# Performance work log

Hardware: AMD Instinct MI355X
Metric: run time of the kernel (lower is better)

## Reference

```python
import jax, jax.numpy as jnp
import numpy as np

N, E, G, F_IN, H, C = 50000, 800000, 512, 128, 96, 10
BN_EPS = 1e-5


def _bn(x, w, b):
    # torch BatchNorm1d training-mode forward: batch stats, biased variance
    mu = jnp.mean(x, axis=0)
    var = jnp.var(x, axis=0)
    return (x - mu) * jax.lax.rsqrt(var + BN_EPS) * w + b


def setup_inputs() -> dict:
    key = jax.random.key(0)
    ks = iter(jax.random.split(key, 64))

    def rn(shape, s=0.05):
        return jax.random.normal(next(ks), shape, jnp.float32) * s

    inp = {
        "x": jax.random.normal(next(ks), (N, F_IN), jnp.float32),
        "edge_index": jax.random.randint(next(ks), (2, E), 0, N, dtype=jnp.int32),
        "batch": jnp.sort(jax.random.randint(next(ks), (N,), 0, G, dtype=jnp.int32)),
        "bn_feat_w": jnp.ones((F_IN,), jnp.float32),
        "bn_feat_b": jnp.full((F_IN,), 1e-4, jnp.float32),
        "Wf": rn((F_IN, H)), "bf": jnp.zeros((H,), jnp.float32),
        "bn_fc_w": jnp.ones((H,), jnp.float32),
        "bn_fc_b": jnp.full((H,), 1e-4, jnp.float32),
        "Wl": rn((H, H)), "bl": jnp.zeros((H,), jnp.float32),
        "bn_hid_w": jnp.ones((H,), jnp.float32),
        "bn_hid_b": jnp.full((H,), 1e-4, jnp.float32),
        "Wc": rn((H, C)), "bc": jnp.zeros((C,), jnp.float32),
    }
    for i in range(3):
        inp[f"W1_{i}"] = rn((H, H)); inp[f"b1_{i}"] = jnp.zeros((H,), jnp.float32)
        inp[f"bnw_{i}"] = jnp.ones((H,), jnp.float32)
        inp[f"bnb_{i}"] = jnp.full((H,), 1e-4, jnp.float32)
        inp[f"W2_{i}"] = rn((H, H)); inp[f"b2_{i}"] = jnp.zeros((H,), jnp.float32)
    return inp


def reference(x, edge_index, batch, bn_feat_w, bn_feat_b, Wf, bf,
              W1_0, b1_0, bnw_0, bnb_0, W2_0, b2_0,
              W1_1, b1_1, bnw_1, bnb_1, W2_1, b2_1,
              W1_2, b1_2, bnw_2, bnb_2, W2_2, b2_2,
              bn_fc_w, bn_fc_b, Wl, bl, bn_hid_w, bn_hid_b, Wc, bc):
    src, dst = edge_index[0], edge_index[1]
    h = _bn(x, bn_feat_w, bn_feat_b)
    # GCNConv(gfn=True): pure linear feature transform, no propagation
    h = jax.nn.relu(h @ Wf + bf)
    gin_params = [
        (W1_0, b1_0, bnw_0, bnb_0, W2_0, b2_0),
        (W1_1, b1_1, bnw_1, bnb_1, W2_1, b2_1),
        (W1_2, b1_2, bnw_2, bnb_2, W2_2, b2_2),
    ]
    for W1, b1, bw, bb, W2, b2 in gin_params:
        # GIN: (1+eps)*x + sum-aggregate of neighbor features (eps=0)
        agg = jax.ops.segment_sum(h[src], dst, num_segments=N)  # [N, H]
        m = h + agg
        m = jax.nn.relu(_bn(m @ W1 + b1, bw, bb))
        h = jax.nn.relu(m @ W2 + b2)
    # global_add_pool over graphs
    g = jax.ops.segment_sum(h, batch, num_segments=G)  # [G, H]
    g = jax.nn.relu(_bn(g, bn_fc_w, bn_fc_b) @ Wl + bl)
    g = _bn(g, bn_hid_w, bn_hid_b)
    logits = g @ Wc + bc
    return jax.nn.log_softmax(logits, axis=-1)
```

## Files before the change

### kernel.cpp

```cpp
#include <hip/hip_runtime.h>

#define N_NODES 50000
#define N_EDGES 800000
#define N_GRAPHS 512
#define F_IN 128
#define HDIM 96
#define NCLS 10
#define BN_EPS 1e-5f

#define NPB 128
#define NBUCK2 ((N_NODES + NPB - 1) / NPB)
#define NEB 128
#define EPB ((N_EDGES + NEB - 1) / NEB)

typedef unsigned int u32;
typedef unsigned short u16;
typedef __attribute__((ext_vector_type(8))) short bf16x8;
typedef __attribute__((ext_vector_type(4))) float f32x4;

__device__ __forceinline__ u16 f2bf(float f) {
    u32 u = __float_as_uint(f);
    u32 r = (u + 0x7fffu + ((u >> 16) & 1u)) >> 16;
    return (u16)r;
}
__device__ __forceinline__ float bflo(u32 w) { return __uint_as_float(w << 16); }
__device__ __forceinline__ float bfhi(u32 w) { return __uint_as_float(w & 0xffff0000u); }
__device__ __forceinline__ float bf2f(u16 v) { return __uint_as_float((u32)v << 16); }

template<int NC>
__global__ __launch_bounds__(256) void colstats4_kernel(const float* __restrict__ in,
                                                        float* __restrict__ partials,
                                                        int nrows) {
    constexpr int CG  = NC / 4;
    constexpr int RPB = 256 / CG;
    const int cg = threadIdx.x % CG;
    const int rg = threadIdx.x / CG;
    float4 s = make_float4(0.f, 0.f, 0.f, 0.f);
    float4 q = make_float4(0.f, 0.f, 0.f, 0.f);
    for (int r = blockIdx.x * RPB + rg; r < nrows; r += gridDim.x * RPB) {
        float4 v = *(const float4*)&in[(size_t)r * NC + cg * 4];
        s.x += v.x; s.y += v.y; s.z += v.z; s.w += v.w;
        q.x += v.x * v.x; q.y += v.y * v.y; q.z += v.z * v.z; q.w += v.w * v.w;
    }
    __shared__ float ss[RPB][NC], sq[RPB][NC];
    *(float4*)&ss[rg][cg * 4] = s;
    *(float4*)&sq[rg][cg * 4] = q;
    __syncthreads();
    if (threadIdx.x < NC) {
        float a = 0.f, b = 0.f;
        #pragma unroll
        for (int r = 0; r < RPB; r++) { a += ss[r][threadIdx.x]; b += sq[r][threadIdx.x]; }
        partials[(size_t)blockIdx.x * 2 * NC + threadIdx.x]      = a;
        partials[(size_t)blockIdx.x * 2 * NC + NC + threadIdx.x] = b;
    }
}

template<int NC>
__global__ __launch_bounds__(2*NC) void colstats_kernel(const float* __restrict__ in,
                                                        float* __restrict__ partials,
                                                        int nrows) {
    const int col  = threadIdx.x % NC;
    const int half = threadIdx.x / NC;
    float s = 0.f, ss = 0.f;
    for (int r = blockIdx.x * 2 + half; r < nrows; r += gridDim.x * 2) {
        float v = in[(size_t)r * NC + col];
        s += v; ss += v * v;
    }
    __shared__ float shs[2][NC], shq[2][NC];
    shs[half][col] = s; shq[half][col] = ss;
    __syncthreads();
    if (half == 0) {
        partials[(size_t)blockIdx.x * 2 * NC + col]      = s  + shs[1][col];
        partials[(size_t)blockIdx.x * 2 * NC + NC + col] = ss + shq[1][col];
    }
}

template<int NCOLS>
__global__ __launch_bounds__(NCOLS * 8) void reduce_finalize_kernel(
        const float* __restrict__ partials, int nslots,
        const float* __restrict__ w,
        const float* __restrict__ b,
        float* __restrict__ ac, float inv_n) {
    const int k   = threadIdx.x % NCOLS;
    const int grp = threadIdx.x / NCOLS;
    const int stride = 2 * NCOLS;
    float s = 0.f, q = 0.f;
    for (int i = grp; i < nslots; i += 8) {
        s += partials[(size_t)i * stride + k];
        q += partials[(size_t)i * stride + NCOLS + k];
    }
    __shared__ float ss[8][NCOLS], sq[8][NCOLS];
    ss[grp][k] = s; sq[grp][k] = q;
    __syncthreads();
    if (grp == 0) {
        float S = ((ss[0][k] + ss[1][k]) + (ss[2][k] + ss[3][k]))
                + ((ss[4][k] + ss[5][k]) + (ss[6][k] + ss[7][k]));
        float Q = ((sq[0][k] + sq[1][k]) + (sq[2][k] + sq[3][k]))
                + ((sq[4][k] + sq[5][k]) + (sq[6][k] + sq[7][k]));
        float mu  = S * inv_n;
        float var = Q * inv_n - mu * mu;
        float a   = w[k] * rsqrtf(var + BN_EPS);
        ac[k]         = a;
        ac[NCOLS + k] = b[k] - mu * a;
    }
}

#define WPF_BLOCKS 48
#define WPH_BLOCKS 36
__global__ __launch_bounds__(256) void wprep_all_kernel(
        const float* __restrict__ Wf, const float* __restrict__ bf, const float* __restrict__ acX,
        const float* __restrict__ W0a, const float* __restrict__ b0a,
        const float* __restrict__ W0b, const float* __restrict__ b0b,
        const float* __restrict__ W1a, const float* __restrict__ b1a,
        const float* __restrict__ W1b, const float* __restrict__ b1b,
        const float* __restrict__ W2a, const float* __restrict__ b2a,
        const float* __restrict__ W2b, const float* __restrict__ b2b,
        u16* __restrict__ wtF, float* __restrict__ bFm,
        u16* __restrict__ wtbase, float* __restrict__ bmbase) {
    const int tid = threadIdx.x;
    int blk = blockIdx.x;
    if (blk < WPF_BLOCKS) {
        int i = blk * 256 + tid;
        if (i < F_IN * 96) {
            int k = i / 96, n = i % 96;
            wtF[n * F_IN + k] = f2bf(Wf[i] * acX[k]);
        }
        if (blk == 0 && tid < 96) {
            float b = bf[tid];
            for (int k = 0; k < F_IN; k++) b += acX[F_IN + k] * Wf[k * 96 + tid];
            bFm[tid] = b;
        }
        return;
    }
    blk -= WPF_BLOCKS;
    const int s  = blk / WPH_BLOCKS;
    const int b2 = blk % WPH_BLOCKS;
    const float* W; const float* bias;
    switch (s) {
        case 0: W = W0a; bias = b0a; break;
        case 1: W = W0b; bias = b0b; break;
        case 2: W = W1a; bias = b1a; break;
        case 3: W = W1b; bias = b1b; break;
        case 4: W = W2a; bias = b2a; break;
        default: W = W2b; bias = b2b; break;
    }
    u16*   wtb  = wtbase + (size_t)s * 96 * HDIM;
    float* bmod = bmbase + (size_t)s * 96;
    int i = b2 * 256 + tid;
    if (i < HDIM * 96) {
        int k = i / 96, n = i % 96;
        wtb[n * HDIM + k] = f2bf(W[i]);
    }
    if (b2 == 0 && tid < 96) bmod[tid] = bias[tid];
}

__global__ __launch_bounds__(1024) void scan1_kernel(const int* __restrict__ in,
                                                     int* __restrict__ tmp,
                                                     int* __restrict__ partial, int n) {
    __shared__ int sh[1024];
    const int i = blockIdx.x * 1024 + threadIdx.x;
    const int d = (i < n) ? in[i] : 0;
    sh[threadIdx.x] = d;
    __syncthreads();
    for (int off = 1; off < 1024; off <<= 1) {
        int v = 0;
        if (threadIdx.x >= off) v = sh[threadIdx.x - off];
        __syncthreads();
        sh[threadIdx.x] += v;
        __syncthreads();
    }
    if (i < n) tmp[i] = sh[threadIdx.x] - d;
    if (threadIdx.x == 1023) partial[blockIdx.x] = sh[1023];
}

__global__ __launch_bounds__(1024) void scan3_rowptr_kernel(const int* __restrict__ tmp,
                                                            const int* __restrict__ partial,
                                                            const int* __restrict__ deg,
                                                            int* __restrict__ row_ptr,
                                                            int n, int nparts) {
    __shared__ int offs;
    if (threadIdx.x < 64) {
        int v = (threadIdx.x < blockIdx.x && threadIdx.x < nparts) ? partial[threadIdx.x] : 0;
        for (int o = 32; o > 0; o >>= 1) v += __shfl_down(v, o, 64);
        if (threadIdx.x == 0) offs = v;
    }
    __syncthreads();
    const int i = blockIdx.x * 1024 + threadIdx.x;
    if (i < n) {
        int v = tmp[i] + offs;
        row_ptr[i] = v;
        if (i == n - 1) row_ptr[n] = v + deg[i];
    }
}

__global__ __launch_bounds__(1024) void scan3_kernel(const int* __restrict__ tmp,
                                                     const int* __restrict__ partial,
                                                     int* __restrict__ out,
                                                     int n, int nparts) {
    __shared__ int offs;
    if (threadIdx.x < 64) {
        int v = (threadIdx.x < blockIdx.x && threadIdx.x < nparts) ? partial[threadIdx.x] : 0;
        for (int o = 32; o > 0; o >>= 1) v += __shfl_down(v, o, 64);
        if (threadIdx.x == 0) offs = v;
    }
    __syncthreads();
    const int i = blockIdx.x * 1024 + threadIdx.x;
    if (i < n) out[i] = tmp[i] + offs;
}

__global__ __launch_bounds__(256) void count_kernel(const int* __restrict__ dst,
                                                    int* __restrict__ deg,
                                                    int* __restrict__ cnt) {
    __shared__ int lc[NBUCK2];
    for (int i = threadIdx.x; i < NBUCK2; i += 256) lc[i] = 0;
    __syncthreads();
    const int lo = blockIdx.x * EPB;
    const int hi = min(lo + EPB, N_EDGES);
    for (int e = lo + threadIdx.x; e < hi; e += 256) {
        int d = dst[e];
        atomicAdd(&lc[d / NPB], 1);
        atomicAdd(&deg[d], 1);
    }
    __syncthreads();
    for (int i = threadIdx.x; i < NBUCK2; i += 256)
        cnt[i * NEB + blockIdx.x] = lc[i];
}

__global__ __launch_bounds__(256) void distribute_kernel(const int* __restrict__ src,
                                                         const int* __restrict__ dst,
                                                         const int* __restrict__ ofs,
                                                         u32* __restrict__ ebuf) {
    __shared__ int lofs[NBUCK2];
    for (int i = threadIdx.x; i < NBUCK2; i += 256) lofs[i] = ofs[i * NEB + blockIdx.x];
    __syncthreads();
    const int lo = blockIdx.x * EPB;
    const int hi = min(lo + EPB, N_EDGES);
    for (int e = lo + threadIdx.x; e < hi; e += 256) {
        int d = dst[e];
        int q = atomicAdd(&lofs[d / NPB], 1);
        ebuf[q] = ((u32)src[e] << 7) | (u32)(d & (NPB - 1));
    }
}

__global__ __launch_bounds__(256) void bucket_fill_kernel(const u32* __restrict__ ebuf,
                                                          const int* __restrict__ ofs,
                                                          const int* __restrict__ row_ptr,
                                                          int* __restrict__ csr) {
    __shared__ int cur[NPB];
    const int p    = blockIdx.x;
    const int base = p * NPB;
    const int nn   = min(NPB, N_NODES - base);
    for (int i = threadIdx.x; i < nn; i += 256) cur[i] = row_ptr[base + i];
    __syncthreads();
    const int e0 = ofs[p * NEB];
    const int e1 = (p + 1 < NBUCK2) ? ofs[(p + 1) * NEB] : N_EDGES;
    for (int e = e0 + threadIdx.x; e < e1; e += 256) {
        u32 v = ebuf[e];
        int pos = atomicAdd(&cur[v & (NPB - 1)], 1);
        csr[pos] = (int)(v >> 7);
    }
}

__device__ __forceinline__ void acc8lo(double& a, u32 w0,u32 w1,u32 w2,u32 w3,u32 w4,u32 w5,u32 w6,u32 w7){
    a += bflo(w0); a += bflo(w1); a += bflo(w2); a += bflo(w3);
    a += bflo(w4); a += bflo(w5); a += bflo(w6); a += bflo(w7);
}
__device__ __forceinline__ void acc8hi(double& a, u32 w0,u32 w1,u32 w2,u32 w3,u32 w4,u32 w5,u32 w6,u32 w7){
    a += bfhi(w0); a += bfhi(w1); a += bfhi(w2); a += bfhi(w3);
    a += bfhi(w4); a += bfhi(w5); a += bfhi(w6); a += bfhi(w7);
}
__global__ __launch_bounds__(192) void agg_kernel(const u16* __restrict__ hb,
                                                  const int* __restrict__ row_ptr,
                                                  const int* __restrict__ csr,
                                                  u16* __restrict__ mb, int n) {
    const int jj   = threadIdx.x % 12;
    const int node = blockIdx.x * 16 + threadIdx.x / 12;
    if (node >= n) return;
    const int p0 = row_ptr[node], p1 = row_ptr[node + 1];
    uint4 sv = *(const uint4*)&hb[(size_t)node * 96 + jj * 8];
    double a0 = bflo(sv.x), a1 = bfhi(sv.x), a2 = bflo(sv.y), a3 = bfhi(sv.y);
    double a4 = bflo(sv.z), a5 = bfhi(sv.z), a6 = bflo(sv.w), a7 = bfhi(sv.w);
    int p = p0;
    for (; p + 8 <= p1; p += 8) {
        int s0 = csr[p],     s1 = csr[p + 1], s2 = csr[p + 2], s3 = csr[p + 3];
        int s4 = csr[p + 4], s5 = csr[p + 5], s6 = csr[p + 6], s7 = csr[p + 7];
        uint4 v0 = *(const uint4*)&hb[(size_t)s0 * 96 + jj * 8];
        uint4 v1 = *(const uint4*)&hb[(size_t)s1 * 96 + jj * 8];
        uint4 v2 = *(const uint4*)&hb[(size_t)s2 * 96 + jj * 8];
        uint4 v3 = *(const uint4*)&hb[(size_t)s3 * 96 + jj * 8];
        uint4 v4 = *(const uint4*)&hb[(size_t)s4 * 96 + jj * 8];
        uint4 v5 = *(const uint4*)&hb[(size_t)s5 * 96 + jj * 8];
        uint4 v6 = *(const uint4*)&hb[(size_t)s6 * 96 + jj * 8];
        uint4 v7 = *(const uint4*)&hb[(size_t)s7 * 96 + jj * 8];
        acc8lo(a0, v0.x,v1.x,v2.x,v3.x,v4.x,v5.x,v6.x,v7.x);
        acc8hi(a1, v0.x,v1.x,v2.x,v3.x,v4.x,v5.x,v6.x,v7.x);
        acc8lo(a2, v0.y,v1.y,v2.y,v3.y,v4.y,v5.y,v6.y,v7.y);
        acc8hi(a3, v0.y,v1.y,v2.y,v3.y,v4.y,v5.y,v6.y,v7.y);
        acc8lo(a4, v0.z,v1.z,v2.z,v3.z,v4.z,v5.z,v6.z,v7.z);
        acc8hi(a5, v0.z,v1.z,v2.z,v3.z,v4.z,v5.z,v6.z,v7.z);
        acc8lo(a6, v0.w,v1.w,v2.w,v3.w,v4.w,v5.w,v6.w,v7.w);
        acc8hi(a7, v0.w,v1.w,v2.w,v3.w,v4.w,v5.w,v6.w,v7.w);
    }
    for (; p < p1; p++) {
        int s = csr[p];
        uint4 v = *(const uint4*)&hb[(size_t)s * 96 + jj * 8];
        a0 += bflo(v.x); a1 += bfhi(v.x); a2 += bflo(v.y); a3 += bfhi(v.y);
        a4 += bflo(v.z); a5 += bfhi(v.z); a6 += bflo(v.w); a7 += bfhi(v.w);
    }
    uint4 o;
    o.x = (u32)f2bf((float)a0) | ((u32)f2bf((float)a1) << 16);
    o.y = (u32)f2bf((float)a2) | ((u32)f2bf((float)a3) << 16);
    o.z = (u32)f2bf((float)a4) | ((u32)f2bf((float)a5) << 16);
    o.w = (u32)f2bf((float)a6) | ((u32)f2bf((float)a7) << 16);
    *(uint4*)&mb[(size_t)node * 96 + jj * 8] = o;
}

template<int KDIM, bool IN_F32, bool IN_AFF_RELU, bool OUT_RELU, bool STATS, bool OUT_BF16>
__global__ __launch_bounds__(256) void mmx_kernel(const void* __restrict__ in_,
                                                  const u16* __restrict__ wt,
                                                  const float* __restrict__ bias,
                                                  const float* __restrict__ ac,
                                                  void* __restrict__ out_,
                                                  float* __restrict__ partials,
                                                  int nrows) {
    constexpr int KP = KDIM + 8;
    constexpr int KB = KDIM / 32;
    __shared__ u16 wlds[96 * KP];
    __shared__ u16 alds[64 * KP];
    __shared__ float sred[2][4][96];
    const int tid = threadIdx.x;

    for (int i = tid; i < 96 * (KDIM / 8); i += 256) {
        int nn = i / (KDIM / 8), c8 = i % (KDIM / 8);
        *(uint4*)&wlds[nn * KP + c8 * 8] = *(const uint4*)&wt[nn * KDIM + c8 * 8];
    }

    const int w    = tid >> 6;
    const int lane = tid & 63;
    const int r16  = lane & 15;
    const int kg   = lane >> 4;
    const int m0   = w * 16;
    float bn[6];
    #pragma unroll
    for (int nt = 0; nt < 6; nt++) bn[nt] = bias[nt * 16 + r16];
    float scol[6] = {0,0,0,0,0,0}, qcol[6] = {0,0,0,0,0,0};

    const int nchunks = (nrows + 63) / 64;
    for (int chunk = blockIdx.x; chunk < nchunks; chunk += gridDim.x) {
        const int row0 = chunk * 64;
        __syncthreads();
        if constexpr (IN_F32) {
            const float* inf = (const float*)in_;
            for (int i = tid; i < 64 * (KDIM / 4); i += 256) {
                int r = i / (KDIM / 4), c4 = i % (KDIM / 4);
                int gr = row0 + r;
                float4 v = (gr < nrows) ? *(const float4*)&inf[(size_t)gr * KDIM + c4 * 4]
                                        : make_float4(0.f, 0.f, 0.f, 0.f);
                if constexpr (IN_AFF_RELU) {
                    float4 a = *(const float4*)&ac[c4 * 4];
                    float4 c = *(const float4*)&ac[KDIM + c4 * 4];
                    v.x = fmaxf(v.x * a.x + c.x, 0.f);
                    v.y = fmaxf(v.y * a.y + c.y, 0.f);
                    v.z = fmaxf(v.z * a.z + c.z, 0.f);
                    v.w = fmaxf(v.w * a.w + c.w, 0.f);
                }
                ushort4 o; o.x = f2bf(v.x); o.y = f2bf(v.y); o.z = f2bf(v.z); o.w = f2bf(v.w);
                *(ushort4*)&alds[r * KP + c4 * 4] = o;
            }
        } else {
            const u16* inb = (const u16*)in_;
            for (int i = tid; i < 64 * (KDIM / 8); i += 256) {
                int r = i / (KDIM / 8), c8 = i % (KDIM / 8);
                int gr = row0 + r;
                uint4 v = (gr < nrows) ? *(const uint4*)&inb[(size_t)gr * KDIM + c8 * 8]
                                       : make_uint4(0u, 0u, 0u, 0u);
                *(uint4*)&alds[r * KP + c8 * 8] = v;
            }
        }
        __syncthreads();

        bf16x8 af[KB];
        #pragma unroll
        for (int kb = 0; kb < KB; kb++)
            af[kb] = *(const bf16x8*)&alds[(m0 + r16) * KP + kb * 32 + kg * 8];

        f32x4 acc[6];
        #pragma unroll
        for (int nt = 0; nt < 6; nt++) acc[nt] = (f32x4){bn[nt], bn[nt], bn[nt], bn[nt]};
        #pragma unroll
        for (int kb = 0; kb < KB; kb++) {
            #pragma unroll
            for (int nt = 0; nt < 6; nt++) {
                bf16x8 bfr = *(const bf16x8*)&wlds[(nt * 16 + r16) * KP + kb * 32 + kg * 8];
                acc[nt] = __builtin_amdgcn_mfma_f32_16x16x32_bf16(af[kb], bfr, acc[nt], 0, 0, 0);
            }
        }

        const int gr0  = row0 + m0 + kg * 4;
        const bool full = (gr0 + 3 < nrows);
        #pragma unroll
        for (int nt = 0; nt < 6; nt++) {
            float v[4] = {acc[nt][0], acc[nt][1], acc[nt][2], acc[nt][3]};
            if constexpr (OUT_RELU) {
                #pragma unroll
                for (int rr = 0; rr < 4; rr++) v[rr] = fmaxf(v[rr], 0.f);
            }
            const int n = nt * 16 + r16;
            #pragma unroll
            for (int rr = 0; rr < 4; rr++) {
                const int gr = gr0 + rr;
                if (full || gr < nrows) {
                    if constexpr (OUT_BF16) ((u16*)out_)[(size_t)gr * 96 + n] = f2bf(v[rr]);
                    else                    ((float*)out_)[(size_t)gr * 96 + n] = v[rr];
                    if constexpr (STATS) { scol[nt] += v[rr]; qcol[nt] += v[rr] * v[rr]; }
                }
            }
        }
    }

    if constexpr (STATS) {
        #pragma unroll
        for (int nt = 0; nt < 6; nt++) {
            scol[nt] += __shfl_xor(scol[nt], 16);
            scol[nt] += __shfl_xor(scol[nt], 32);
            qcol[nt] += __shfl_xor(qcol[nt], 16);
            qcol[nt] += __shfl_xor(qcol[nt], 32);
        }
        __syncthreads();
        if (kg == 0) {
            #pragma unroll
            for (int nt = 0; nt < 6; nt++) {
                sred[0][w][nt * 16 + r16] = scol[nt];
                sred[1][w][nt * 16 + r16] = qcol[nt];
            }
        }
        __syncthreads();
        if (tid < 96) {
            float a = (sred[0][0][tid] + sred[0][1][tid]) + (sred[0][2][tid] + sred[0][3][tid]);
            float b = (sred[1][0][tid] + sred[1][1][tid]) + (sred[1][2][tid] + sred[1][3][tid]);
            partials[(size_t)blockIdx.x * 192 + tid]      = a;
            partials[(size_t)blockIdx.x * 192 + 96 + tid] = b;
        }
    }
}

__device__ __forceinline__ int lower_bound_dev(const int* __restrict__ a, int n, int v) {
    int lo = 0, hi = n;
    while (lo < hi) { int m = (lo + hi) >> 1; if (a[m] < v) lo = m + 1; else hi = m; }
    return lo;
}
__global__ __launch_bounds__(96) void pool_det_kernel(const u16* __restrict__ hb,
                                                      const int* __restrict__ batch,
                                                      float* __restrict__ g) {
    const int gi = blockIdx.x;
    __shared__ int sh_lo, sh_hi;
    if (threadIdx.x == 0) sh_lo = lower_bound_dev(batch, N_NODES, gi);
    if (threadIdx.x == 1) sh_hi = lower_bound_dev(batch, N_NODES, gi + 1);
    __syncthreads();
    const int lo = sh_lo, hi = sh_hi;
    const int j = threadIdx.x;
    float s0 = 0.f, s1 = 0.f, s2 = 0.f, s3 = 0.f;
    int r = lo;
    for (; r + 4 <= hi; r += 4) {
        s0 += bf2f(hb[(size_t)r       * 96 + j]);
        s1 += bf2f(hb[(size_t)(r + 1) * 96 + j]);
        s2 += bf2f(hb[(size_t)(r + 2) * 96 + j]);
        s3 += bf2f(hb[(size_t)(r + 3) * 96 + j]);
    }
    for (; r < hi; r++) s0 += bf2f(hb[(size_t)r * 96 + j]);
    g[(size_t)gi * 96 + j] = (s0 + s1) + (s2 + s3);
}

template<int KDIM, bool IN_AFF, bool IN_RELU, bool OUT_RELU, bool STATS>
__global__ __launch_bounds__(192) void mm_kernel(const float* __restrict__ in,
                                                 const float* __restrict__ W,
                                                 const float* __restrict__ bias,
                                                 const float* __restrict__ ac,
                                                 float* __restrict__ out,
                                                 float* __restrict__ partials, int nrows) {
    constexpr int KG = KDIM / 4;
    __shared__ float ws[KDIM][96];
    __shared__ float xs[32][KDIM];
    const int tid = threadIdx.x;
    const int cg  = tid % 24;
    const int rg  = tid / 24;
    for (int i = tid; i < KDIM * 24; i += 192) {
        int k = i / 24, c4 = i % 24;
        *(float4*)&ws[k][c4 * 4] = *(const float4*)&W[(size_t)k * 96 + c4 * 4];
    }
    const float4 bj = *(const float4*)&bias[cg * 4];
    float s0=0,s1=0,s2=0,s3=0, q0=0,q1=0,q2=0,q3=0;
    const int nchunks = (nrows + 31) / 32;
    for (int chunk = blockIdx.x; chunk < nchunks; chunk += gridDim.x) {
        const int row0 = chunk * 32;
        __syncthreads();
        for (int i = tid; i < 32 * KG; i += 192) {
            int r = i / KG, g = i % KG;
            int gr = row0 + r;
            float4 v = make_float4(0.f, 0.f, 0.f, 0.f);
            if (gr < nrows) v = *(const float4*)&in[(size_t)gr * KDIM + g * 4];
            if constexpr (IN_AFF) {
                float4 a = *(const float4*)&ac[g * 4];
                float4 c = *(const float4*)&ac[KDIM + g * 4];
                v.x = v.x * a.x + c.x; v.y = v.y * a.y + c.y;
                v.z = v.z * a.z + c.z; v.w = v.w * a.w + c.w;
            }
            if constexpr (IN_RELU) {
                v.x = fmaxf(v.x, 0.f); v.y = fmaxf(v.y, 0.f);
                v.z = fmaxf(v.z, 0.f); v.w = fmaxf(v.w, 0.f);
            }
            *(float4*)&xs[r][4 * (g ^ (r & 7))] = v;
        }
        __syncthreads();
        float acc[4][4];
        #pragma unroll
        for (int m = 0; m < 4; m++) {
            acc[m][0] = bj.x; acc[m][1] = bj.y; acc[m][2] = bj.z; acc[m][3] = bj.w;
        }
        #pragma unroll 4
        for (int g = 0; g < KG; g++) {
            const int xi = 4 * (g ^ rg);
            float4 xv0 = *(const float4*)&xs[rg     ][xi];
            float4 xv1 = *(const float4*)&xs[rg +  8][xi];
            float4 xv2 = *(const float4*)&xs[rg + 16][xi];
            float4 xv3 = *(const float4*)&xs[rg + 24][xi];
            #pragma unroll
            for (int i = 0; i < 4; i++) {
                float4 wv = *(const float4*)&ws[g * 4 + i][cg * 4];
                float x0 = (i==0)?xv0.x:(i==1)?xv0.y:(i==2)?xv0.z:xv0.w;
                float x1 = (i==0)?xv1.x:(i==1)?xv1.y:(i==2)?xv1.z:xv1.w;
                float x2 = (i==0)?xv2.x:(i==1)?xv2.y:(i==2)?xv2.z:xv2.w;
                float x3 = (i==0)?xv3.x:(i==1)?xv3.y:(i==2)?xv3.z:xv3.w;
                acc[0][0] = fmaf(x0, wv.x, acc[0][0]); acc[0][1] = fmaf(x0, wv.y, acc[0][1]);
                acc[0][2] = fmaf(x0, wv.z, acc[0][2]); acc[0][3] = fmaf(x0, wv.w, acc[0][3]);
                acc[1][0] = fmaf(x1, wv.x, acc[1][0]); acc[1][1] = fmaf(x1, wv.y, acc[1][1]);
                acc[1][2] = fmaf(x1, wv.z, acc[1][2]); acc[1][3] = fmaf(x1, wv.w, acc[1][3]);
                acc[2][0] = fmaf(x2, wv.x, acc[2][0]); acc[2][1] = fmaf(x2, wv.y, acc[2][1]);
                acc[2][2] = fmaf(x2, wv.z, acc[2][2]); acc[2][3] = fmaf(x2, wv.w, acc[2][3]);
                acc[3][0] = fmaf(x3, wv.x, acc[3][0]); acc[3][1] = fmaf(x3, wv.y, acc[3][1]);
                acc[3][2] = fmaf(x3, wv.z, acc[3][2]); acc[3][3] = fmaf(x3, wv.w, acc[3][3]);
            }
        }
        #pragma unroll
        for (int m = 0; m < 4; m++) {
            const int gr = row0 + rg + 8 * m;
            if (gr < nrows) {
                float4 o = make_float4(acc[m][0], acc[m][1], acc[m][2], acc[m][3]);
                if constexpr (OUT_RELU) {
                    o.x = fmaxf(o.x, 0.f); o.y = fmaxf(o.y, 0.f);
                    o.z = fmaxf(o.z, 0.f); o.w = fmaxf(o.w, 0.f);
                }
                *(float4*)&out[(size_t)gr * 96 + cg * 4] = o;
                if constexpr (STATS) {
                    s0 += o.x; q0 += o.x * o.x; s1 += o.y; q1 += o.y * o.y;
                    s2 += o.z; q2 += o.z * o.z; s3 += o.w; q3 += o.w * o.w;
                }
            }
        }
    }
    if constexpr (STATS) {
        __syncthreads();
        float* rs = &xs[0][0];
        float* rq = rs + 8 * 96;
        rs[rg * 96 + cg * 4 + 0] = s0; rs[rg * 96 + cg * 4 + 1] = s1;
        rs[rg * 96 + cg * 4 + 2] = s2; rs[rg * 96 + cg * 4 + 3] = s3;
        rq[rg * 96 + cg * 4 + 0] = q0; rq[rg * 96 + cg * 4 + 1] = q1;
        rq[rg * 96 + cg * 4 + 2] = q2; rq[rg * 96 + cg * 4 + 3] = q3;
        __syncthreads();
        if (tid < 96) {
            float a = 0.f, b = 0.f;
            #pragma unroll
            for (int r = 0; r < 8; r++) { a += rs[r * 96 + tid]; b += rq[r * 96 + tid]; }
            partials[(size_t)blockIdx.x * 192 + tid]      = a;
            partials[(size_t)blockIdx.x * 192 + 96 + tid] = b;
        }
    }
}

__global__ void head_kernel(const float* __restrict__ g1, const float* __restrict__ ac,
                            const float* __restrict__ Wc, const float* __restrict__ bc,
                            float* __restrict__ out, int ngraphs) {
    int gi = blockIdx.x * blockDim.x + threadIdx.x;
    if (gi >= ngraphs) return;
    float v[NCLS];
    #pragma unroll
    for (int c = 0; c < NCLS; c++) v[c] = bc[c];
    for (int k = 0; k < HDIM; k++) {
        float x = g1[(size_t)gi * HDIM + k] * ac[k] + ac[HDIM + k];
        #pragma unroll
        for (int c = 0; c < NCLS; c++) v[c] = fmaf(x, Wc[k * NCLS + c], v[c]);
    }
    float mx = v[0];
    #pragma unroll
    for (int c = 1; c < NCLS; c++) mx = fmaxf(mx, v[c]);
    float sum = 0.f;
    #pragma unroll
    for (int c = 0; c < NCLS; c++) sum += expf(v[c] - mx);
    float lse = mx + logf(sum);
    #pragma unroll
    for (int c = 0; c < NCLS; c++) out[(size_t)gi * NCLS + c] = v[c] - lse;
}

extern "C" void kernel_launch(void* const* d_in, const int* in_sizes, int n_in,
                              void* d_out, int out_size, void* d_ws, size_t ws_size,
                              hipStream_t stream) {
    const float* x         = (const float*)d_in[0];
    const int*   ei        = (const int*)  d_in[1];
    const int*   batch     = (const int*)  d_in[2];
    const float* bn_feat_w = (const float*)d_in[3];
    const float* bn_feat_b = (const float*)d_in[4];
    const float* Wf        = (const float*)d_in[5];
    const float* bfv       = (const float*)d_in[6];
    const float* bn_fc_w   = (const float*)d_in[7];
    const float* bn_fc_b   = (const float*)d_in[8];
    const float* Wl        = (const float*)d_in[9];
    const float* bl        = (const float*)d_in[10];
    const float* bn_hid_w  = (const float*)d_in[11];
    const float* bn_hid_b  = (const float*)d_in[12];
    const float* Wc        = (const float*)d_in[13];
    const float* bc        = (const float*)d_in[14];
    float* out = (float*)d_out;

    char* p = (char*)d_ws;
    auto alloc = [&](size_t bytes) { char* q = p; p += (bytes + 255) & ~(size_t)255; return q; };

    int*   deg    = (int*)  alloc((size_t)N_NODES * 4);

    float* pstatX = (float*)alloc((size_t)256 * 2 * F_IN * 4);
    float* pstatT = (float*)alloc((size_t)1024 * 192 * 4);
    float* pstatG = (float*)alloc((size_t)64 * 192 * 4);
    float* pstatG1= (float*)alloc((size_t)16 * 192 * 4);

    u16*   hb     = (u16*)  alloc((size_t)N_NODES * HDIM * 2);
    u16*   mb     = (u16*)  alloc((size_t)N_NODES * HDIM * 2);
    float* tf     = (float*)alloc((size_t)N_NODES * HDIM * 4);
    float* g      = (float*)alloc((size_t)N_GRAPHS * HDIM * 4);
    float* g1     = (float*)alloc((size_t)N_GRAPHS * HDIM * 4);
    float* acX    = (float*)alloc(2 * F_IN * 4);
    float* acT    = (float*)alloc(2 * HDIM * 4);
    float* acG    = (float*)alloc(2 * HDIM * 4);
    float* acHid  = (float*)alloc(2 * HDIM * 4);
    u16*   wtF    = (u16*)  alloc(96 * F_IN * 2);
    float* bFmod  = (float*)alloc(96 * 4);
    u16*   wtH    = (u16*)  alloc((size_t)6 * 96 * HDIM * 2);
    float* bmH    = (float*)alloc((size_t)6 * 96 * 4);
    int* row_ptr  = (int*)alloc((size_t)(N_NODES + 1) * 4);
    int* csr      = (int*)alloc((size_t)N_EDGES * 4);
    int* stmp     = (int*)alloc((size_t)N_NODES * 4);
    int* spart    = (int*)alloc(64 * 4);
    int* cnt      = (int*)alloc((size_t)NBUCK2 * NEB * 4);
    int* ofs      = (int*)alloc((size_t)NBUCK2 * NEB * 4);
    int* stmp2    = (int*)alloc((size_t)NBUCK2 * NEB * 4);
    int* spart2   = (int*)alloc(64 * 4);
    u32* ebuf     = (u32*)alloc((size_t)N_EDGES * 4);

    const int* srcp = ei;
    const int* dstp = ei + N_EDGES;

    const int nch64  = (N_NODES + 63) / 64;
    const int gridF  = (nch64 < 768) ? nch64 : 768;
    const int grid96 = (nch64 < 1024) ? nch64 : 1024;
    const int gridG  = (N_GRAPHS + 31) / 32;
    const int nscan  = (N_NODES + 1023) / 1024;
    const int ncb    = NBUCK2 * NEB;
    const int nscan2 = (ncb + 1023) / 1024;

    hipMemsetAsync(deg, 0, (size_t)N_NODES * 4, stream);

    colstats4_kernel<F_IN><<<256, 256, 0, stream>>>(x, pstatX, N_NODES);
    reduce_finalize_kernel<F_IN><<<1, F_IN * 8, 0, stream>>>(pstatX, 256, bn_feat_w, bn_feat_b, acX, 1.0f / N_NODES);
    wprep_all_kernel<<<WPF_BLOCKS + 6 * WPH_BLOCKS, 256, 0, stream>>>(
        Wf, bfv, acX,
        (const float*)d_in[15], (const float*)d_in[16],
        (const float*)d_in[19], (const float*)d_in[20],
        (const float*)d_in[21], (const float*)d_in[22],
        (const float*)d_in[25], (const float*)d_in[26],
        (const float*)d_in[27], (const float*)d_in[28],
        (const float*)d_in[31], (const float*)d_in[32],
        wtF, bFmod, wtH, bmH);
    mmx_kernel<F_IN, true, false, true, false, true><<<gridF, 256, 0, stream>>>(x, wtF, bFmod, nullptr, hb, nullptr, N_NODES);

    count_kernel<<<NEB, 256, 0, stream>>>(dstp, deg, cnt);
    scan1_kernel<<<nscan, 1024, 0, stream>>>(deg, stmp, spart, N_NODES);
    scan3_rowptr_kernel<<<nscan, 1024, 0, stream>>>(stmp, spart, deg, row_ptr, N_NODES, nscan);
    scan1_kernel<<<nscan2, 1024, 0, stream>>>(cnt, stmp2, spart2, ncb);
    scan3_kernel<<<nscan2, 1024, 0, stream>>>(stmp2, spart2, ofs, ncb, nscan2);
    distribute_kernel<<<NEB, 256, 0, stream>>>(srcp, dstp, ofs, ebuf);
    bucket_fill_kernel<<<NBUCK2, 256, 0, stream>>>(ebuf, ofs, row_ptr, csr);

    for (int l = 0; l < 3; l++) {
        const float* bw = (const float*)d_in[17 + 6 * l];
        const float* bb = (const float*)d_in[18 + 6 * l];
        u16*   wt1 = wtH + (size_t)(2 * l)     * 96 * HDIM;
        u16*   wt2 = wtH + (size_t)(2 * l + 1) * 96 * HDIM;
        float* b1m = bmH + (size_t)(2 * l)     * 96;
        float* b2m = bmH + (size_t)(2 * l + 1) * 96;
        agg_kernel<<<(N_NODES + 15) / 16, 192, 0, stream>>>(hb, row_ptr, csr, mb, N_NODES);
        mmx_kernel<HDIM, false, false, false, true, false><<<grid96, 256, 0, stream>>>(mb, wt1, b1m, nullptr, tf, pstatT, N_NODES);
        reduce_finalize_kernel<HDIM><<<1, HDIM * 8, 0, stream>>>(pstatT, grid96, bw, bb, acT, 1.0f / N_NODES);
        mmx_kernel<HDIM, true, true, true, false, true><<<grid96, 256, 0, stream>>>(tf, wt2, b2m, acT, hb, nullptr, N_NODES);
    }

    pool_det_kernel<<<N_GRAPHS, 96, 0, stream>>>(hb, batch, g);

    colstats_kernel<HDIM><<<64, 2 * HDIM, 0, stream>>>(g, pstatG, N_GRAPHS);
    reduce_finalize_kernel<HDIM><<<1, HDIM * 8, 0, stream>>>(pstatG, 64, bn_fc_w, bn_fc_b, acG, 1.0f / N_GRAPHS);
    mm_kernel<HDIM, true, false, true, true><<<gridG, 192, 0, stream>>>(g, Wl, bl, acG, g1, pstatG1, N_GRAPHS);
    reduce_finalize_kernel<HDIM><<<1, HDIM * 8, 0, stream>>>(pstatG1, gridG, bn_hid_w, bn_hid_b, acHid, 1.0f / N_GRAPHS);

    head_kernel<<<2, 256, 0, stream>>>(g1, acHid, Wc, bc, out, N_GRAPHS);
}
```

Measured before the change: 395.0 us.

## Fuse neighbor aggregation into first GIN matmul, merge scans and pool stats

Neighbor sum-aggregation now runs inside the first per-layer MFMA matmul kernel. Each block gathers a 64-row tile into LDS and multiplies it directly, which removes the bf16 intermediate buffer write/read and one launch per layer. The two prefix scans are merged into shared launches, and graph pooling now emits per-graph BN partials, which removes the separate colstats kernel. The trade-off is that the gather is now limited to the matmul grid size and cannot overlap with the MFMA phase inside a block, so latency hiding may drop.

```diff
diff --git a/kernel.cpp b/kernel.cpp
--- a/kernel.cpp
+++ b/kernel.cpp
@@ -52,26 +52,6 @@
         for (int r = 0; r < RPB; r++) { a += ss[r][threadIdx.x]; b += sq[r][threadIdx.x]; }
         partials[(size_t)blockIdx.x * 2 * NC + threadIdx.x]      = a;
         partials[(size_t)blockIdx.x * 2 * NC + NC + threadIdx.x] = b;
-    }
-}
-
-template<int NC>
-__global__ __launch_bounds__(2*NC) void colstats_kernel(const float* __restrict__ in,
-                                                        float* __restrict__ partials,
-                                                        int nrows) {
-    const int col  = threadIdx.x % NC;
-    const int half = threadIdx.x / NC;
-    float s = 0.f, ss = 0.f;
-    for (int r = blockIdx.x * 2 + half; r < nrows; r += gridDim.x * 2) {
-        float v = in[(size_t)r * NC + col];
-        s += v; ss += v * v;
-    }
-    __shared__ float shs[2][NC], shq[2][NC];
-    shs[half][col] = s; shq[half][col] = ss;
-    __syncthreads();
-    if (half == 0) {
-        partials[(size_t)blockIdx.x * 2 * NC + col]      = s  + shs[1][col];
-        partials[(size_t)blockIdx.x * 2 * NC + NC + col] = ss + shq[1][col];
     }
 }
 
@@ -154,11 +134,15 @@
     if (b2 == 0 && tid < 96) bmod[tid] = bias[tid];
 }
 
-__global__ __launch_bounds__(1024) void scan1_kernel(const int* __restrict__ in,
-                                                     int* __restrict__ tmp,
-                                                     int* __restrict__ partial, int n) {
+__global__ __launch_bounds__(1024) void scan1_fused_kernel(
+        const int* __restrict__ inA, int nA, int* __restrict__ tmpA, int* __restrict__ partA,
+        const int* __restrict__ inB, int nB, int* __restrict__ tmpB, int* __restrict__ partB,
+        int nblkA) {
+    const int* in; int n; int* tmp; int* partial; int base;
+    if ((int)blockIdx.x < nblkA) { in = inA; n = nA; tmp = tmpA; partial = partA; base = blockIdx.x; }
+    else                         { in = inB; n = nB; tmp = tmpB; partial = partB; base = blockIdx.x - nblkA; }
     __shared__ int sh[1024];
-    const int i = blockIdx.x * 1024 + threadIdx.x;
+    const int i = base * 1024 + threadIdx.x;
     const int d = (i < n) ? in[i] : 0;
     sh[threadIdx.x] = d;
     __syncthreads();
@@ -170,42 +154,34 @@
         __syncthreads();
     }
     if (i < n) tmp[i] = sh[threadIdx.x] - d;
-    if (threadIdx.x == 1023) partial[blockIdx.x] = sh[1023];
-}
-
-__global__ __launch_bounds__(1024) void scan3_rowptr_kernel(const int* __restrict__ tmp,
-                                                            const int* __restrict__ partial,
-                                                            const int* __restrict__ deg,
-                                                            int* __restrict__ row_ptr,
-                                                            int n, int nparts) {
+    if (threadIdx.x == 1023) partial[base] = sh[1023];
+}
+
+__global__ __launch_bounds__(1024) void scan3_fused_kernel(
+        const int* __restrict__ tmpA, const int* __restrict__ partA,
+        const int* __restrict__ degA, int* __restrict__ row_ptr, int nA, int npA,
+        const int* __restrict__ tmpB, const int* __restrict__ partB,
+        int* __restrict__ ofs, int nB, int npB, int nblkA) {
+    const int* tmp; const int* partial; int n, nparts, base; bool isA;
+    if ((int)blockIdx.x < nblkA) { tmp = tmpA; partial = partA; n = nA; nparts = npA; base = blockIdx.x; isA = true; }
+    else                         { tmp = tmpB; partial = partB; n = nB; nparts = npB; base = blockIdx.x - nblkA; isA = false; }
     __shared__ int offs;
     if (threadIdx.x < 64) {
-        int v = (threadIdx.x < blockIdx.x && threadIdx.x < nparts) ? partial[threadIdx.x] : 0;
+        int v = (threadIdx.x < base && (int)threadIdx.x < nparts) ? partial[threadIdx.x] : 0;
         for (int o = 32; o > 0; o >>= 1) v += __shfl_down(v, o, 64);
         if (threadIdx.x == 0) offs = v;
     }
     __syncthreads();
-    const int i = blockIdx.x * 1024 + threadIdx.x;
+    const int i = base * 1024 + threadIdx.x;
     if (i < n) {
         int v = tmp[i] + offs;
-        row_ptr[i] = v;
-        if (i == n - 1) row_ptr[n] = v + deg[i];
-    }
-}
-
-__global__ __launch_bounds__(1024) void scan3_kernel(const int* __restrict__ tmp,
-                                                     const int* __restrict__ partial,
-                                                     int* __restrict__ out,
-                                                     int n, int nparts) {
-    __shared__ int offs;
-    if (threadIdx.x < 64) {
-        int v = (threadIdx.x < blockIdx.x && threadIdx.x < nparts) ? partial[threadIdx.x] : 0;
-        for (int o = 32; o > 0; o >>= 1) v += __shfl_down(v, o, 64);
-        if (threadIdx.x == 0) offs = v;
-    }
-    __syncthreads();
-    const int i = blockIdx.x * 1024 + threadIdx.x;
-    if (i < n) out[i] = tmp[i] + offs;
+        if (isA) {
+            row_ptr[i] = v;
+            if (i == n - 1) row_ptr[n] = v + degA[i];
+        } else {
+            ofs[i] = v;
+        }
+    }
 }
 
 __global__ __launch_bounds__(256) void count_kernel(const int* __restrict__ dst,
@@ -261,58 +237,136 @@
     }
 }
 
-__device__ __forceinline__ void acc8lo(double& a, u32 w0,u32 w1,u32 w2,u32 w3,u32 w4,u32 w5,u32 w6,u32 w7){
-    a += bflo(w0); a += bflo(w1); a += bflo(w2); a += bflo(w3);
-    a += bflo(w4); a += bflo(w5); a += bflo(w6); a += bflo(w7);
-}
-__device__ __forceinline__ void acc8hi(double& a, u32 w0,u32 w1,u32 w2,u32 w3,u32 w4,u32 w5,u32 w6,u32 w7){
-    a += bfhi(w0); a += bfhi(w1); a += bfhi(w2); a += bfhi(w3);
-    a += bfhi(w4); a += bfhi(w5); a += bfhi(w6); a += bfhi(w7);
-}
-__global__ __launch_bounds__(192) void agg_kernel(const u16* __restrict__ hb,
-                                                  const int* __restrict__ row_ptr,
-                                                  const int* __restrict__ csr,
-                                                  u16* __restrict__ mb, int n) {
-    const int jj   = threadIdx.x % 12;
-    const int node = blockIdx.x * 16 + threadIdx.x / 12;
-    if (node >= n) return;
-    const int p0 = row_ptr[node], p1 = row_ptr[node + 1];
-    uint4 sv = *(const uint4*)&hb[(size_t)node * 96 + jj * 8];
-    double a0 = bflo(sv.x), a1 = bfhi(sv.x), a2 = bflo(sv.y), a3 = bfhi(sv.y);
-    double a4 = bflo(sv.z), a5 = bfhi(sv.z), a6 = bflo(sv.w), a7 = bfhi(sv.w);
-    int p = p0;
-    for (; p + 8 <= p1; p += 8) {
-        int s0 = csr[p],     s1 = csr[p + 1], s2 = csr[p + 2], s3 = csr[p + 3];
-        int s4 = csr[p + 4], s5 = csr[p + 5], s6 = csr[p + 6], s7 = csr[p + 7];
-        uint4 v0 = *(const uint4*)&hb[(size_t)s0 * 96 + jj * 8];
-        uint4 v1 = *(const uint4*)&hb[(size_t)s1 * 96 + jj * 8];
-        uint4 v2 = *(const uint4*)&hb[(size_t)s2 * 96 + jj * 8];
-        uint4 v3 = *(const uint4*)&hb[(size_t)s3 * 96 + jj * 8];
-        uint4 v4 = *(const uint4*)&hb[(size_t)s4 * 96 + jj * 8];
-        uint4 v5 = *(const uint4*)&hb[(size_t)s5 * 96 + jj * 8];
-        uint4 v6 = *(const uint4*)&hb[(size_t)s6 * 96 + jj * 8];
-        uint4 v7 = *(const uint4*)&hb[(size_t)s7 * 96 + jj * 8];
-        acc8lo(a0, v0.x,v1.x,v2.x,v3.x,v4.x,v5.x,v6.x,v7.x);
-        acc8hi(a1, v0.x,v1.x,v2.x,v3.x,v4.x,v5.x,v6.x,v7.x);
-        acc8lo(a2, v0.y,v1.y,v2.y,v3.y,v4.y,v5.y,v6.y,v7.y);
-        acc8hi(a3, v0.y,v1.y,v2.y,v3.y,v4.y,v5.y,v6.y,v7.y);
-        acc8lo(a4, v0.z,v1.z,v2.z,v3.z,v4.z,v5.z,v6.z,v7.z);
-        acc8hi(a5, v0.z,v1.z,v2.z,v3.z,v4.z,v5.z,v6.z,v7.z);
-        acc8lo(a6, v0.w,v1.w,v2.w,v3.w,v4.w,v5.w,v6.w,v7.w);
-        acc8hi(a7, v0.w,v1.w,v2.w,v3.w,v4.w,v5.w,v6.w,v7.w);
-    }
-    for (; p < p1; p++) {
-        int s = csr[p];
-        uint4 v = *(const uint4*)&hb[(size_t)s * 96 + jj * 8];
-        a0 += bflo(v.x); a1 += bfhi(v.x); a2 += bflo(v.y); a3 += bfhi(v.y);
-        a4 += bflo(v.z); a5 += bfhi(v.z); a6 += bflo(v.w); a7 += bfhi(v.w);
-    }
-    uint4 o;
-    o.x = (u32)f2bf((float)a0) | ((u32)f2bf((float)a1) << 16);
-    o.y = (u32)f2bf((float)a2) | ((u32)f2bf((float)a3) << 16);
-    o.z = (u32)f2bf((float)a4) | ((u32)f2bf((float)a5) << 16);
-    o.w = (u32)f2bf((float)a6) | ((u32)f2bf((float)a7) << 16);
-    *(uint4*)&mb[(size_t)node * 96 + jj * 8] = o;
+__global__ __launch_bounds__(256) void aggmm_kernel(const u16* __restrict__ hb,
+                                                    const int* __restrict__ row_ptr,
+                                                    const int* __restrict__ csr,
+                                                    const u16* __restrict__ wt,
+                                                    const float* __restrict__ bias,
+                                                    float* __restrict__ tf,
+                                                    float* __restrict__ partials,
+                                                    int nrows) {
+    constexpr int KP = HDIM + 8;
+    constexpr int KB = HDIM / 32;
+    __shared__ u16 wlds[96 * KP];
+    __shared__ u16 alds[64 * KP];
+    __shared__ float sred[2][4][96];
+    const int tid = threadIdx.x;
+
+    for (int i = tid; i < 96 * (HDIM / 8); i += 256) {
+        int nn = i / (HDIM / 8), c8 = i % (HDIM / 8);
+        *(uint4*)&wlds[nn * KP + c8 * 8] = *(const uint4*)&wt[nn * HDIM + c8 * 8];
+    }
+
+    const int w    = tid >> 6;
+    const int lane = tid & 63;
+    const int r16  = lane & 15;
+    const int kg   = lane >> 4;
+    const int m0   = w * 16;
+    float bn[6];
+    #pragma unroll
+    for (int nt = 0; nt < 6; nt++) bn[nt] = bias[nt * 16 + r16];
+    float scol[6] = {0,0,0,0,0,0}, qcol[6] = {0,0,0,0,0,0};
+
+    const int nchunks = (nrows + 63) / 64;
+    for (int chunk = blockIdx.x; chunk < nchunks; chunk += gridDim.x) {
+        const int row0 = chunk * 64;
+        __syncthreads();
+        for (int t = tid; t < 64 * 12; t += 256) {
+            const int r  = t / 12, sl = t % 12;
+            const int node = row0 + r;
+            uint4 ov = make_uint4(0u, 0u, 0u, 0u);
+            if (node < nrows) {
+                const int p0 = row_ptr[node], p1 = row_ptr[node + 1];
+                uint4 sv = *(const uint4*)&hb[(size_t)node * 96 + sl * 8];
+                double a0 = bflo(sv.x), a1 = bfhi(sv.x), a2 = bflo(sv.y), a3 = bfhi(sv.y);
+                double a4 = bflo(sv.z), a5 = bfhi(sv.z), a6 = bflo(sv.w), a7 = bfhi(sv.w);
+                int p = p0;
+                for (; p + 4 <= p1; p += 4) {
+                    int s0 = csr[p], s1 = csr[p + 1], s2 = csr[p + 2], s3 = csr[p + 3];
+                    uint4 v0 = *(const uint4*)&hb[(size_t)s0 * 96 + sl * 8];
+                    uint4 v1 = *(const uint4*)&hb[(size_t)s1 * 96 + sl * 8];
+                    uint4 v2 = *(const uint4*)&hb[(size_t)s2 * 96 + sl * 8];
+                    uint4 v3 = *(const uint4*)&hb[(size_t)s3 * 96 + sl * 8];
+                    a0 += bflo(v0.x); a0 += bflo(v1.x); a0 += bflo(v2.x); a0 += bflo(v3.x);
+                    a1 += bfhi(v0.x); a1 += bfhi(v1.x); a1 += bfhi(v2.x); a1 += bfhi(v3.x);
+                    a2 += bflo(v0.y); a2 += bflo(v1.y); a2 += bflo(v2.y); a2 += bflo(v3.y);
+                    a3 += bfhi(v0.y); a3 += bfhi(v1.y); a3 += bfhi(v2.y); a3 += bfhi(v3.y);
+                    a4 += bflo(v0.z); a4 += bflo(v1.z); a4 += bflo(v2.z); a4 += bflo(v3.z);
+                    a5 += bfhi(v0.z); a5 += bfhi(v1.z); a5 += bfhi(v2.z); a5 += bfhi(v3.z);
+                    a6 += bflo(v0.w); a6 += bflo(v1.w); a6 += bflo(v2.w); a6 += bflo(v3.w);
+                    a7 += bfhi(v0.w); a7 += bfhi(v1.w); a7 += bfhi(v2.w); a7 += bfhi(v3.w);
+                }
+                for (; p < p1; p++) {
+                    int s = csr[p];
+                    uint4 v = *(const uint4*)&hb[(size_t)s * 96 + sl * 8];
+                    a0 += bflo(v.x); a1 += bfhi(v.x); a2 += bflo(v.y); a3 += bfhi(v.y);
+                    a4 += bflo(v.z); a5 += bfhi(v.z); a6 += bflo(v.w); a7 += bfhi(v.w);
+                }
+                ov.x = (u32)f2bf((float)a0) | ((u32)f2bf((float)a1) << 16);
+                ov.y = (u32)f2bf((float)a2) | ((u32)f2bf((float)a3) << 16);
+                ov.z = (u32)f2bf((float)a4) | ((u32)f2bf((float)a5) << 16);
+                ov.w = (u32)f2bf((float)a6) | ((u32)f2bf((float)a7) << 16);
+            }
+            *(uint4*)&alds[r * KP + sl * 8] = ov;
+        }
+        __syncthreads();
+
+        bf16x8 af[KB];
+        #pragma unroll
+        for (int kb = 0; kb < KB; kb++)
+            af[kb] = *(const bf16x8*)&alds[(m0 + r16) * KP + kb * 32 + kg * 8];
+
+        f32x4 acc[6];
+        #pragma unroll
+        for (int nt = 0; nt < 6; nt++) acc[nt] = (f32x4){bn[nt], bn[nt], bn[nt], bn[nt]};
+        #pragma unroll
+        for (int kb = 0; kb < KB; kb++) {
+            #pragma unroll
+            for (int nt = 0; nt < 6; nt++) {
+                bf16x8 bfr = *(const bf16x8*)&wlds[(nt * 16 + r16) * KP + kb * 32 + kg * 8];
+                acc[nt] = __builtin_amdgcn_mfma_f32_16x16x32_bf16(af[kb], bfr, acc[nt], 0, 0, 0);
+            }
+        }
+
+        const int gr0  = row0 + m0 + kg * 4;
+        const bool full = (gr0 + 3 < nrows);
+        #pragma unroll
+        for (int nt = 0; nt < 6; nt++) {
+            const int n = nt * 16 + r16;
+            #pragma unroll
+            for (int rr = 0; rr < 4; rr++) {
+                const int gr = gr0 + rr;
+                if (full || gr < nrows) {
+                    float v = acc[nt][rr];
+                    tf[(size_t)gr * 96 + n] = v;
+                    scol[nt] += v; qcol[nt] += v * v;
+                }
+            }
+        }
+    }
+
+    #pragma unroll
+    for (int nt = 0; nt < 6; nt++) {
+        scol[nt] += __shfl_xor(scol[nt], 16);
+        scol[nt] += __shfl_xor(scol[nt], 32);
+        qcol[nt] += __shfl_xor(qcol[nt], 16);
+        qcol[nt] += __shfl_xor(qcol[nt], 32);
+    }
+    __syncthreads();
+    if (kg == 0) {
+        #pragma unroll
+        for (int nt = 0; nt < 6; nt++) {
+            sred[0][w][nt * 16 + r16] = scol[nt];
+            sred[1][w][nt * 16 + r16] = qcol[nt];
+        }
+    }
+    __syncthreads();
+    if (tid < 96) {
+        float a = (sred[0][0][tid] + sred[0][1][tid]) + (sred[0][2][tid] + sred[0][3][tid]);
+        float b = (sred[1][0][tid] + sred[1][1][tid]) + (sred[1][2][tid] + sred[1][3][tid]);
+        partials[(size_t)blockIdx.x * 192 + tid]      = a;
+        partials[(size_t)blockIdx.x * 192 + 96 + tid] = b;
+    }
 }
 
 template<int KDIM, bool IN_F32, bool IN_AFF_RELU, bool OUT_RELU, bool STATS, bool OUT_BF16>
@@ -449,9 +503,10 @@
     while (lo < hi) { int m = (lo + hi) >> 1; if (a[m] < v) lo = m + 1; else hi = m; }
     return lo;
 }
-__global__ __launch_bounds__(96) void pool_det_kernel(const u16* __restrict__ hb,
-                                                      const int* __restrict__ batch,
-                                                      float* __restrict__ g) {
+__global__ __launch_bounds__(96) void pool_stats_kernel(const u16* __restrict__ hb,
+                                                        const int* __restrict__ batch,
+                                                        float* __restrict__ g,
+                                                        float* __restrict__ partials) {
     const int gi = blockIdx.x;
     __shared__ int sh_lo, sh_hi;
     if (threadIdx.x == 0) sh_lo = lower_bound_dev(batch, N_NODES, gi);
@@ -468,7 +523,10 @@
         s3 += bf2f(hb[(size_t)(r + 3) * 96 + j]);
     }
     for (; r < hi; r++) s0 += bf2f(hb[(size_t)r * 96 + j]);
-    g[(size_t)gi * 96 + j] = (s0 + s1) + (s2 + s3);
+    float val = (s0 + s1) + (s2 + s3);
+    g[(size_t)gi * 96 + j] = val;
+    partials[(size_t)gi * 192 + j]      = val;
+    partials[(size_t)gi * 192 + 96 + j] = val * val;
 }
 
 template<int KDIM, bool IN_AFF, bool IN_RELU, bool OUT_RELU, bool STATS>
@@ -628,11 +686,10 @@
 
     float* pstatX = (float*)alloc((size_t)256 * 2 * F_IN * 4);
     float* pstatT = (float*)alloc((size_t)1024 * 192 * 4);
-    float* pstatG = (float*)alloc((size_t)64 * 192 * 4);
+    float* pstatG = (float*)alloc((size_t)N_GRAPHS * 192 * 4);
     float* pstatG1= (float*)alloc((size_t)16 * 192 * 4);
 
     u16*   hb     = (u16*)  alloc((size_t)N_NODES * HDIM * 2);
-    u16*   mb     = (u16*)  alloc((size_t)N_NODES * HDIM * 2);
     float* tf     = (float*)alloc((size_t)N_NODES * HDIM * 4);
     float* g      = (float*)alloc((size_t)N_GRAPHS * HDIM * 4);
     float* g1     = (float*)alloc((size_t)N_GRAPHS * HDIM * 4);
@@ -681,10 +738,10 @@
     mmx_kernel<F_IN, true, false, true, false, true><<<gridF, 256, 0, stream>>>(x, wtF, bFmod, nullptr, hb, nullptr, N_NODES);
 
     count_kernel<<<NEB, 256, 0, stream>>>(dstp, deg, cnt);
-    scan1_kernel<<<nscan, 1024, 0, stream>>>(deg, stmp, spart, N_NODES);
-    scan3_rowptr_kernel<<<nscan, 1024, 0, stream>>>(stmp, spart, deg, row_ptr, N_NODES, nscan);
-    scan1_kernel<<<nscan2, 1024, 0, stream>>>(cnt, stmp2, spart2, ncb);
-    scan3_kernel<<<nscan2, 1024, 0, stream>>>(stmp2, spart2, ofs, ncb, nscan2);
+    scan1_fused_kernel<<<nscan + nscan2, 1024, 0, stream>>>(deg, N_NODES, stmp, spart,
+                                                            cnt, ncb, stmp2, spart2, nscan);
+    scan3_fused_kernel<<<nscan + nscan2, 1024, 0, stream>>>(stmp, spart, deg, row_ptr, N_NODES, nscan,
+                                                            stmp2, spart2, ofs, ncb, nscan2, nscan);
     distribute_kernel<<<NEB, 256, 0, stream>>>(srcp, dstp, ofs, ebuf);
     bucket_fill_kernel<<<NBUCK2, 256, 0, stream>>>(ebuf, ofs, row_ptr, csr);
 
@@ -695,16 +752,13 @@
         u16*   wt2 = wtH + (size_t)(2 * l + 1) * 96 * HDIM;
         float* b1m = bmH + (size_t)(2 * l)     * 96;
         float* b2m = bmH + (size_t)(2 * l + 1) * 96;
-        agg_kernel<<<(N_NODES + 15) / 16, 192, 0, stream>>>(hb, row_ptr, csr, mb, N_NODES);
-        mmx_kernel<HDIM, false, false, false, true, false><<<grid96, 256, 0, stream>>>(mb, wt1, b1m, nullptr, tf, pstatT, N_NODES);
+        aggmm_kernel<<<grid96, 256, 0, stream>>>(hb, row_ptr, csr, wt1, b1m, tf, pstatT, N_NODES);
         reduce_finalize_kernel<HDIM><<<1, HDIM * 8, 0, stream>>>(pstatT, grid96, bw, bb, acT, 1.0f / N_NODES);
         mmx_kernel<HDIM, true, true, true, false, true><<<grid96, 256, 0, stream>>>(tf, wt2, b2m, acT, hb, nullptr, N_NODES);
     }
 
-    pool_det_kernel<<<N_GRAPHS, 96, 0, stream>>>(hb, batch, g);
-
-    colstats_kernel<HDIM><<<64, 2 * HDIM, 0, stream>>>(g, pstatG, N_GRAPHS);
-    reduce_finalize_kernel<HDIM><<<1, HDIM * 8, 0, stream>>>(pstatG, 64, bn_fc_w, bn_fc_b, acG, 1.0f / N_GRAPHS);
+    pool_stats_kernel<<<N_GRAPHS, 96, 0, stream>>>(hb, batch, g, pstatG);
+    reduce_finalize_kernel<HDIM><<<1, HDIM * 8, 0, stream>>>(pstatG, N_GRAPHS, bn_fc_w, bn_fc_b, acG, 1.0f / N_GRAPHS);
     mm_kernel<HDIM, true, false, true, true><<<gridG, 192, 0, stream>>>(g, Wl, bl, acG, g1, pstatG1, N_GRAPHS);
     reduce_finalize_kernel<HDIM><<<1, HDIM * 8, 0, stream>>>(pstatG1, gridG, bn_hid_w, bn_hid_b, acHid, 1.0f / N_GRAPHS);
 
```

Result: no change. 392.3 us (-0.7%).
